# Optimization experiments

Hardware: AMD Instinct MI355X
Metric: run time of the kernel (lower is better)

The kernel has to match this reference:

```python
import jax, jax.numpy as jnp
import numpy as np

N = 8192       # nodes == in_channels (diff matrix is NxN)
DF = 256       # feature dim of z
E = 65536      # edges (unused by forward, kept for signature fidelity)
M = 4096       # len(reliable_negatives)
NEG = 10       # neg_samples
STEPS = 10     # num_diffusion_steps
TEMP = 0.2


def setup_inputs() -> dict:
    key = jax.random.key(0)
    k1, k2, k3, k4, k5 = jax.random.split(key, 5)
    z = jax.random.normal(k1, (N, DF), dtype=jnp.float32)
    # learned parameter; init positive-uniform so row sums are well conditioned
    diff_matrix = jax.random.uniform(k2, (N, N), dtype=jnp.float32)
    edge_index = jax.random.randint(k3, (2, E), 0, N)
    reliable_negatives = jax.random.randint(k4, (M,), 0, N)
    # deterministic stand-in for torch.randint(0, len(reliable_negatives), (neg_samples,))
    neg_idx = jax.random.randint(k5, (NEG,), 0, M)
    return {"z": z, "diff_matrix": diff_matrix, "edge_index": edge_index,
            "reliable_negatives": reliable_negatives, "neg_idx": neg_idx}


def _l2norm(x):
    # F.normalize(dim=1): divide by L2 norm clamped at 1e-12
    n = jnp.sqrt(jnp.sum(x * x, axis=1, keepdims=True))
    return x / jnp.maximum(n, 1e-12)


def reference(z, diff_matrix, edge_index, reliable_negatives, neg_idx):
    # 10-step loop: mm(inverse(diag(rowsum)), M) == row-wise reciprocal scaling
    dm = diff_matrix
    for _ in range(STEPS):
        dm = dm / jnp.sum(dm, axis=1, keepdims=True)  # [N, N]
    # (normalized_diff_matrix with +eps*I is computed in the original but unused)

    anchor = z                       # [N, DF]
    positive = dm @ z                # [N, DF] diffused features
    negative = z[neg_idx]            # [NEG, DF]

    a = _l2norm(anchor)
    p = _l2norm(positive)
    n = _l2norm(negative)

    pos_sim = jnp.sum(a * p, axis=1) / TEMP                 # [N]
    neg_sim = jnp.exp(jnp.einsum('nd,kd->nk', a, n) / TEMP)  # [N, NEG]
    loss = -jnp.log(jnp.exp(pos_sim) / (jnp.exp(pos_sim) + neg_sim.sum(axis=1))).mean()
    return loss
```

## Files before the change

kernel.cpp:

```cpp
#include <hip/hip_runtime.h>
#include <hip/hip_bf16.h>


typedef float f32x4 __attribute__((ext_vector_type(4)));
typedef short s16x8 __attribute__((ext_vector_type(8)));

#define NN 8192
#define DFF 256
#define NNEG 10

__device__ __forceinline__ unsigned short f2bf(float x) {
  return __builtin_bit_cast(unsigned short, __float2bfloat16(x));
}

__device__ __forceinline__ float bf2f(unsigned short u) {
  return __builtin_bit_cast(float, (unsigned int)u << 16);
}

__device__ __forceinline__ void gload_lds16(const void* g, void* l) {
  __builtin_amdgcn_global_load_lds(
      (const __attribute__((address_space(1))) void*)(void*)g,
      (__attribute__((address_space(3))) void*)l, 16, 0, 0);
}

__device__ __forceinline__ float dot4(float4 a, float4 b) {
  return a.x * b.x + a.y * b.y + a.z * b.z + a.w * b.w;
}

__global__ void k_pack(const float* __restrict__ z,
                       unsigned short* __restrict__ zp) {
  __shared__ float tile[64][65];
  const int bx = blockIdx.x;
  const int by = blockIdx.y;
  const int t = threadIdx.x;
  const int lc = t & 63, lq = t >> 6;
#pragma unroll
  for (int p = 0; p < 16; ++p) {
    const int kr = lq * 16 + p;
    tile[kr][lc] = z[(size_t)(bx * 64 + kr) * DFF + by * 64 + lc];
  }
  __syncthreads();
#pragma unroll
  for (int p2 = 0; p2 < 2; ++p2) {
    const int ko = lq * 2 + p2;
    s16x8 v;
#pragma unroll
    for (int ke = 0; ke < 8; ++ke) v[ke] = (short)f2bf(tile[ko * 8 + ke][lc]);
    const int chunk = bx * 2 + (ko >> 2);
    const int kw = ko & 3;
    const int d = by * 64 + lc;
    *(s16x8*)(zp + (size_t)chunk * 8192 + kw * 2048 + d * 8) = v;
  }
}

__global__ __launch_bounds__(512, 2) void k_gemm(const float* __restrict__ dm,
                                                 const unsigned short* __restrict__ zp,
                                                 unsigned short* __restrict__ part,
                                                 int KS) {
  __shared__ __align__(16) unsigned short sA[2][4096];
  __shared__ __align__(16) unsigned short sB[2][8192];
  const int bx = blockIdx.x;
  const int ks = bx & (KS - 1);
  const int mtile = bx / KS;
  const int klen = NN / KS;
  const int k0 = ks * klen;
  const int c0 = k0 >> 5;
  const int steps = klen / 32;
  const int tid = threadIdx.x;
  const int w = tid >> 6;
  const int l = tid & 63;
  const int m0 = mtile * 128;

  const int arow = w * 16 + (l & 15);
  const int akw = l >> 4;
  const float* asrc = dm + (size_t)(m0 + arow) * NN + k0 + akw * 8;

  const int r16 = l & 15, kw = l >> 4;
  const int wm = w >> 2, wn = w & 3;

  f32x4 acc[4][4] = {};
  f32x4 a0, a1;

#define LOAD_A(t_)                                                            \
  {                                                                           \
    a0 = __builtin_nontemporal_load((const f32x4*)(asrc + (t_)*32));          \
    a1 = __builtin_nontemporal_load((const f32x4*)(asrc + (t_)*32 + 4));      \
  }

#define WRITE_A(s_)                                                          \
  {                                                                          \
    s16x8 h_;                                                                \
    h_[0] = (short)f2bf(a0[0]); h_[1] = (short)f2bf(a0[1]);                  \
    h_[2] = (short)f2bf(a0[2]); h_[3] = (short)f2bf(a0[3]);                  \
    h_[4] = (short)f2bf(a1[0]); h_[5] = (short)f2bf(a1[1]);                  \
    h_[6] = (short)f2bf(a1[2]); h_[7] = (short)f2bf(a1[3]);                  \
    *(s16x8*)&sA[s_][akw * 1024 + arow * 8] = h_;                            \
  }

#define STAGE_B(t_, s_)                                                      \
  {                                                                          \
    const unsigned short* cs_ = zp + (size_t)(c0 + (t_)) * 8192;             \
    _Pragma("unroll") for (int q = 0; q < 2; ++q) {                          \
      const int piece_ = w * 2 + q;                     \
      gload_lds16((const char*)(cs_ + piece_ * 512) + l * 16,                \
                  (char*)sB[s_] + piece_ * 1024);                            \
    }                                                                        \
  }

#define COMPUTE(s_)                                                          \
  {                                                                          \
    s16x8 af[4], bfr[4];                                                     \
    _Pragma("unroll") for (int mi = 0; mi < 4; ++mi) {                       \
      const int row_ = wm * 64 + mi * 16 + r16;                              \
      af[mi] = *(const s16x8*)&sA[s_][kw * 1024 + row_ * 8];                 \
    }                                                                        \
    _Pragma("unroll") for (int nj = 0; nj < 4; ++nj) {                       \
      const int col_ = wn * 64 + nj * 16 + r16;                              \
      bfr[nj] = *(const s16x8*)&sB[s_][kw * 2048 + col_ * 8];                \
    }                                                                        \
    _Pragma("unroll") for (int mi = 0; mi < 4; ++mi)                         \
      _Pragma("unroll") for (int nj = 0; nj < 4; ++nj)                       \
        acc[mi][nj] = __builtin_amdgcn_mfma_f32_16x16x32_bf16(               \
            af[mi], bfr[nj], acc[mi][nj], 0, 0, 0);                          \
  }

  STAGE_B(0, 0);
  LOAD_A(0);
  WRITE_A(0);
  __syncthreads();

  for (int t = 0; t < steps; ++t) {
    const int cur = t & 1, nxt = cur ^ 1;
    if (t + 1 < steps) {
      LOAD_A(t + 1);
      STAGE_B(t + 1, nxt);
    }
    COMPUTE(cur);
    if (t + 1 < steps) WRITE_A(nxt);
    __syncthreads();
  }

#undef LOAD_A
#undef WRITE_A
#undef STAGE_B
#undef COMPUTE

  unsigned short* cb = part + (size_t)ks * NN * DFF;
#pragma unroll
  for (int mi = 0; mi < 4; ++mi)
#pragma unroll
    for (int nj = 0; nj < 4; ++nj) {
      const int col = wn * 64 + nj * 16 + r16;
      const int row0 = m0 + wm * 64 + mi * 16 + kw * 4;
#pragma unroll
      for (int r = 0; r < 4; ++r)
        cb[(size_t)(row0 + r) * DFF + col] = f2bf(acc[mi][nj][r]);
    }
}

__global__ __launch_bounds__(256) void k_loss(const float* __restrict__ z,
                                              const unsigned short* __restrict__ part,
                                              const int* __restrict__ neg_idx,
                                              float* __restrict__ lpart, int KS) {
  __shared__ float sneg[NNEG * DFF];
  __shared__ float swsum[4];
  const int t = threadIdx.x;
  const int w = t >> 6, l = t & 63;
  for (int k = w; k < NNEG; k += 4) {
    const int idx = neg_idx[k];
    float4 v = *(const float4*)(z + (size_t)idx * DFF + l * 4);
    float ss = dot4(v, v);
#pragma unroll
    for (int off = 32; off > 0; off >>= 1) ss += __shfl_xor(ss, off);
    const float s = 1.0f / fmaxf(sqrtf(ss), 1e-12f);
    float4 o;
    o.x = v.x * s; o.y = v.y * s; o.z = v.z * s; o.w = v.w * s;
    *(float4*)&sneg[k * DFF + l * 4] = o;
  }
  __syncthreads();
  const int gw = blockIdx.x * 4 + w;
  float lsum = 0.f;
  for (int rr = 0; rr < 8; ++rr) {
    const int i = gw * 8 + rr;
    const float4 a = *(const float4*)(z + (size_t)i * DFF + l * 4);
    float4 p; p.x = 0.f; p.y = 0.f; p.z = 0.f; p.w = 0.f;
    for (int ksp = 0; ksp < KS; ++ksp) {
      const ushort4 q =
          *(const ushort4*)(part + ((size_t)ksp * NN + i) * DFF + l * 4);
      p.x += bf2f(q.x); p.y += bf2f(q.y); p.z += bf2f(q.z); p.w += bf2f(q.w);
    }
    float vals[13];
    vals[0] = dot4(a, a);
    vals[1] = dot4(p, p);
    vals[2] = dot4(a, p);
#pragma unroll
    for (int k = 0; k < NNEG; ++k) {
      const float4 nv = *(const float4*)&sneg[k * DFF + l * 4];
      vals[3 + k] = dot4(a, nv);
    }
#pragma unroll
    for (int off = 32; off > 0; off >>= 1)
#pragma unroll
      for (int j = 0; j < 13; ++j) vals[j] += __shfl_xor(vals[j], off);
    const float na = fmaxf(sqrtf(vals[0]), 1e-12f);
    const float npp = fmaxf(sqrtf(vals[1]), 1e-12f);
    const float ps = vals[2] / (na * npp) * 5.0f;
    float S = 0.f;
#pragma unroll
    for (int k = 0; k < NNEG; ++k) S += expf(vals[3 + k] / na * 5.0f);
    lsum += logf(expf(ps) + S) - ps;
  }
  if (l == 0) swsum[w] = lsum;
  __syncthreads();
  if (t == 0) lpart[blockIdx.x] = swsum[0] + swsum[1] + swsum[2] + swsum[3];
}

__global__ void k_final(const float* __restrict__ lpart, float* __restrict__ out) {
  const int t = threadIdx.x;
  float v = lpart[t] + lpart[t + 64] + lpart[t + 128] + lpart[t + 192];
#pragma unroll
  for (int off = 32; off > 0; off >>= 1) v += __shfl_xor(v, off);
  if (t == 0) out[0] = v * (1.0f / (float)NN);
}

extern "C" void kernel_launch(void* const* d_in, const int* in_sizes, int n_in,
                              void* d_out, int out_size, void* d_ws, size_t ws_size,
                              hipStream_t stream) {
  const float* z = (const float*)d_in[0];
  const float* dm = (const float*)d_in[1];
  const int* neg_idx = (const int*)d_in[4];
  float* out = (float*)d_out;

  const size_t ZP = (size_t)NN * DFF * 2;
  auto need = [ZP](size_t ks) { return ZP + ks * (size_t)NN * DFF * 2 + 1024; };
  int KS = 8;
  if (ws_size < need(8)) KS = (ws_size >= need(4)) ? 4 : 2;

  char* ws = (char*)d_ws;
  unsigned short* zp = (unsigned short*)ws;
  unsigned short* part = (unsigned short*)(ws + ZP);
  float* lpart = (float*)(ws + ZP + (size_t)KS * NN * DFF * 2);

  k_pack<<<dim3(128, 4), 256, 0, stream>>>(z, zp);
  k_gemm<<<64 * KS, 512, 0, stream>>>(dm, zp, part, KS);
  k_loss<<<256, 256, 0, stream>>>(z, part, neg_idx, lpart, KS);
  k_final<<<1, 64, 0, stream>>>(lpart, out);
}
```

Baseline: 136.6 us.

## Stage fp32 A tiles directly into LDS via global_load_lds with swizzle

The dm tile is now loaded straight into LDS as fp32 through global_load_lds, in an XOR-swizzled layout, instead of going through registers and being converted to bf16 before the LDS write. The bf16 conversion moves into the compute phase after the LDS read. The block-to-tile mapping changes so that consecutive blocks share a K-split, and launch bounds ask for 4 blocks per CU. This removes register staging and conversion from the load path, but doubles the A tile's LDS footprint, adds conversion work inside the MFMA loop, and hardcodes 64 m-tiles in the block index mapping.

```diff
diff --git a/kernel.cpp b/kernel.cpp
--- a/kernel.cpp
+++ b/kernel.cpp
@@ -53,15 +53,15 @@
   }
 }
 
-__global__ __launch_bounds__(512, 2) void k_gemm(const float* __restrict__ dm,
+__global__ __launch_bounds__(512, 4) void k_gemm(const float* __restrict__ dm,
                                                  const unsigned short* __restrict__ zp,
                                                  unsigned short* __restrict__ part,
                                                  int KS) {
-  __shared__ __align__(16) unsigned short sA[2][4096];
+  __shared__ __align__(16) char sA[2][16384];
   __shared__ __align__(16) unsigned short sB[2][8192];
   const int bx = blockIdx.x;
-  const int ks = bx & (KS - 1);
-  const int mtile = bx / KS;
+  const int mtile = bx & 63;
+  const int ks = bx >> 6;
   const int klen = NN / KS;
   const int k0 = ks * klen;
   const int c0 = k0 >> 5;
@@ -71,30 +71,25 @@
   const int l = tid & 63;
   const int m0 = mtile * 128;
 
-  const int arow = w * 16 + (l & 15);
-  const int akw = l >> 4;
-  const float* asrc = dm + (size_t)(m0 + arow) * NN + k0 + akw * 8;
-
   const int r16 = l & 15, kw = l >> 4;
   const int wm = w >> 2, wn = w & 3;
 
+  const int o0 = w * 128 + l, o1 = o0 + 64;
+  const int kws0 = o0 >> 8, sp0 = o0 & 255;
+  const int kws1 = o1 >> 8, sp1 = o1 & 255;
+  const int s0 = sp0 ^ ((sp0 >> 3) & 7);
+  const int s1 = sp1 ^ ((sp1 >> 3) & 7);
+  const float* a0src =
+      dm + (size_t)(m0 + (s0 >> 1)) * NN + k0 + kws0 * 8 + (s0 & 1) * 4;
+  const float* a1src =
+      dm + (size_t)(m0 + (s1 >> 1)) * NN + k0 + kws1 * 8 + (s1 & 1) * 4;
+
   f32x4 acc[4][4] = {};
-  f32x4 a0, a1;
-
-#define LOAD_A(t_)                                                            \
-  {                                                                           \
-    a0 = __builtin_nontemporal_load((const f32x4*)(asrc + (t_)*32));          \
-    a1 = __builtin_nontemporal_load((const f32x4*)(asrc + (t_)*32 + 4));      \
-  }
-
-#define WRITE_A(s_)                                                          \
+
+#define STAGE_A(t_, s_)                                                      \
   {                                                                          \
-    s16x8 h_;                                                                \
-    h_[0] = (short)f2bf(a0[0]); h_[1] = (short)f2bf(a0[1]);                  \
-    h_[2] = (short)f2bf(a0[2]); h_[3] = (short)f2bf(a0[3]);                  \
-    h_[4] = (short)f2bf(a1[0]); h_[5] = (short)f2bf(a1[1]);                  \
-    h_[6] = (short)f2bf(a1[2]); h_[7] = (short)f2bf(a1[3]);                  \
-    *(s16x8*)&sA[s_][akw * 1024 + arow * 8] = h_;                            \
+    gload_lds16(a0src + (t_)*32, sA[s_] + o0 * 16);                          \
+    gload_lds16(a1src + (t_)*32, sA[s_] + o1 * 16);                          \
   }
 
 #define STAGE_B(t_, s_)                                                      \
@@ -111,8 +106,18 @@
   {                                                                          \
     s16x8 af[4], bfr[4];                                                     \
     _Pragma("unroll") for (int mi = 0; mi < 4; ++mi) {                       \
-      const int row_ = wm * 64 + mi * 16 + r16;                              \
-      af[mi] = *(const s16x8*)&sA[s_][kw * 1024 + row_ * 8];                 \
+      const int row_ = wm * 64 + mi * 16 + r16;                  \
+      const int m_ = (row_ >> 2) & 7;                                        \
+      const int sa_ = (2 * row_) ^ m_;                    \
+      const int sb2_ = sa_ ^ 1;                           \
+      const f32x4 x0 = *(const f32x4*)(sA[s_] + kw * 4096 + sa_ * 16);       \
+      const f32x4 x1 = *(const f32x4*)(sA[s_] + kw * 4096 + sb2_ * 16);      \
+      s16x8 h_;                                                              \
+      h_[0] = (short)f2bf(x0[0]); h_[1] = (short)f2bf(x0[1]);                \
+      h_[2] = (short)f2bf(x0[2]); h_[3] = (short)f2bf(x0[3]);                \
+      h_[4] = (short)f2bf(x1[0]); h_[5] = (short)f2bf(x1[1]);                \
+      h_[6] = (short)f2bf(x1[2]); h_[7] = (short)f2bf(x1[3]);                \
+      af[mi] = h_;                                                           \
     }                                                                        \
     _Pragma("unroll") for (int nj = 0; nj < 4; ++nj) {                       \
       const int col_ = wn * 64 + nj * 16 + r16;                              \
@@ -124,24 +129,21 @@
             af[mi], bfr[nj], acc[mi][nj], 0, 0, 0);                          \
   }
 
+  STAGE_A(0, 0);
   STAGE_B(0, 0);
-  LOAD_A(0);
-  WRITE_A(0);
   __syncthreads();
 
   for (int t = 0; t < steps; ++t) {
     const int cur = t & 1, nxt = cur ^ 1;
     if (t + 1 < steps) {
-      LOAD_A(t + 1);
+      STAGE_A(t + 1, nxt);
       STAGE_B(t + 1, nxt);
     }
     COMPUTE(cur);
-    if (t + 1 < steps) WRITE_A(nxt);
     __syncthreads();
   }
 
-#undef LOAD_A
-#undef WRITE_A
+#undef STAGE_A
 #undef STAGE_B
 #undef COMPUTE
 
```

Result: faster. 129.4 us (-5.3%).
